# Performance work log

Measured on AMD Instinct MI355X. Metric: run time of the kernel, lower is better.

## Reference

```python
import jax, jax.numpy as jnp
import numpy as np

B, S, D, H = 1, 2048, 1024, 16
DEPTH = D // H          # 64
A_DFF = 1024
NRES = 2                # num_reslayerA
SLOPE = 0.2             # LeakyReLU slope in plga attention
POW_EPS = 1e-9


def _ln(x, g, b):
    m = jnp.mean(x, axis=-1, keepdims=True)
    v = jnp.var(x, axis=-1, keepdims=True)
    return (x - m) * jax.lax.rsqrt(v + 1e-6) * g + b


def setup_inputs() -> dict:
    key = jax.random.key(0)
    ks = jax.random.split(key, 12)
    s = 0.02
    W = lambda k, shp: jax.random.normal(k, shp, jnp.float32) * s
    return {
        'q': jax.random.normal(ks[0], (B, S, D), jnp.float32),
        'k': jax.random.normal(ks[1], (B, S, D), jnp.float32),
        'v': jax.random.normal(ks[2], (B, S, D), jnp.float32),
        'mask': jnp.zeros((B, 1, 1, S), jnp.float32),
        'wq_w': W(ks[3], (D, D)), 'wq_b': jnp.zeros((D,), jnp.float32),
        'wk_w': W(ks[4], (D, D)), 'wk_b': jnp.zeros((D,), jnp.float32),
        'wv_w': W(ks[5], (D, D)), 'wv_b': jnp.zeros((D,), jnp.float32),
        'wo_w': W(ks[6], (D, D)), 'wo_b': jnp.zeros((D,), jnp.float32),
        # stacked ResLayerA params: Dense(depth->A_dff, relu) -> Dense(A_dff->depth) -> LN
        'rl_w1': W(ks[7], (NRES, DEPTH, A_DFF)), 'rl_b1': jnp.zeros((NRES, A_DFF), jnp.float32),
        'rl_w2': W(ks[8], (NRES, A_DFF, DEPTH)), 'rl_b2': jnp.zeros((NRES, DEPTH), jnp.float32),
        'rl_g': jnp.ones((NRES, DEPTH), jnp.float32), 'rl_beta': jnp.zeros((NRES, DEPTH), jnp.float32),
        # plga layer params: power coefficients, attention vector, bias
        'pw': jnp.ones((DEPTH,), jnp.float32),
        'a_vec': W(ks[9], (DEPTH,)),
        'ba': jnp.zeros((), jnp.float32),
    }


def reference(q, k, v, mask, wq_w, wq_b, wk_w, wk_b, wv_w, wv_b, wo_w, wo_b,
              rl_w1, rl_b1, rl_w2, rl_b2, rl_g, rl_beta, pw, a_vec, ba):
    Bq = q.shape[0]
    split = lambda x: x.reshape(Bq, -1, H, DEPTH).transpose(0, 2, 1, 3)  # [b,h,s,d]
    qh = split(q @ wq_w + wq_b)
    kh = split(k @ wk_w + wk_b)
    vh = split(v @ wv_w + wv_b)

    # metric tensor A = q^T q  -> [b,h,depth,depth]
    A = jnp.einsum('bhsd,bhse->bhde', qh, qh)
    # ResLayerA residual dense+LN stack over last dim
    for i in range(NRES):
        Ain = A
        hdn = jax.nn.relu(A @ rl_w1[i] + rl_b1[i])
        A = _ln((hdn @ rl_w2[i] + rl_b2[i]) + Ain, rl_g[i], rl_beta[i])

    # power-law graph attention (plga_layer, att_head=1, activation=None)
    Ap = jnp.power(jnp.abs(A) + POW_EPS, pw)                  # element-wise learned power
    avAp = jnp.einsum('d,bhde->bhe', a_vec, Ap)               # [b,h,depth] per-dim scaling
    E = jnp.einsum('bhsd,bhd,bhtd->bhst', qh, avAp, kh)       # pairwise logits [b,h,s,s]
    Ep = jnp.where(E > 0, E, SLOPE * E) + ba                  # LeakyReLU + learned bias
    Ep = Ep + mask * (-1e9)
    attv = jax.nn.softmax(Ep, axis=-1)
    Hnext = jnp.einsum('bhst,bhtd->bhsd', attv, vh)

    Hnext = Hnext.transpose(0, 2, 1, 3).reshape(Bq, -1, D)
    out = Hnext @ wo_w + wo_b
    return (out, E, A, pw, attv, ba, avAp, Ep)
```

## Files before the change

### kernel.cpp

```cpp
#include <hip/hip_runtime.h>
#include <stdint.h>

#define S_ 2048
#define D_ 1024
#define H_ 16
#define DEP_ 64

typedef float f32x4 __attribute__((ext_vector_type(4)));
typedef __bf16 bf16x8 __attribute__((ext_vector_type(8)));

#define MFMA16(a,b,c) __builtin_amdgcn_mfma_f32_16x16x32_bf16((a),(b),(c),0,0,0)

static constexpr size_t OFF_E    = 2097152ull;
static constexpr size_t OFF_A    = 69206016ull;
static constexpr size_t OFF_PW   = 69271552ull;
static constexpr size_t OFF_ATT  = 69271616ull;
static constexpr size_t OFF_BA   = 136380480ull;
static constexpr size_t OFF_AVAP = 136380481ull;
static constexpr size_t OFF_EP   = 136381505ull;

__device__ __forceinline__ short f2b(float f) {
  union { float f; uint32_t u; } c; c.f = f;
  uint32_t u = c.u;
  uint32_t r = (u + 0x7fffu + ((u >> 16) & 1u)) >> 16;
  return (short)(r & 0xffffu);
}
__device__ __forceinline__ float b2f(short s) {
  union { uint32_t u; float f; } c; c.u = ((uint32_t)(uint16_t)s) << 16;
  return c.f;
}
__device__ __forceinline__ void st_nt(float* p, f32x4 v) {
  __builtin_nontemporal_store(v, (f32x4*)p);
}

__global__ void k_cvt_all(const float* __restrict__ q, const float* __restrict__ k,
                          const float* __restrict__ v, const float* __restrict__ wq,
                          const float* __restrict__ wk, const float* __restrict__ wv,
                          const float* __restrict__ wo, const float* __restrict__ w1,
                          const float* __restrict__ w2, short* __restrict__ xbf,
                          short* __restrict__ wT, short* __restrict__ w1T,
                          short* __restrict__ w2T) {
  __shared__ float tile[64][65];
  int bid = blockIdx.x, t = threadIdx.x;
  if (bid < 6144) {
    int z = bid >> 11, bx = bid & 2047;
    const float* src = (z == 0) ? q : (z == 1) ? k : v;
    short* d = xbf + (size_t)z * (S_*D_);
    int i = (bx*256 + t)*4;
    float4 f = *(const float4*)(src + i);
    short4 o;
    o.x = f2b(f.x); o.y = f2b(f.y); o.z = f2b(f.z); o.w = f2b(f.w);
    *(short4*)(d + i) = o;
  } else if (bid < 7168) {
    int u = bid - 6144, z = u >> 8, tl = u & 255;
    int k0 = (tl >> 4)*64, n0 = (tl & 15)*64;
    const float* W = (z == 0) ? wq : (z == 1) ? wk : (z == 2) ? wv : wo;
    short* d = wT + (size_t)z * (D_*D_);
    for (int i = 0; i < 16; ++i) {
      int e = i*256 + t, r = e >> 6, c = e & 63;
      tile[r][c] = W[(size_t)(k0+r)*D_ + n0 + c];
    }
    __syncthreads();
    for (int i = 0; i < 16; ++i) {
      int e = i*256 + t, r = e >> 6, c = e & 63;
      d[(size_t)(n0+r)*D_ + k0 + c] = f2b(tile[c][r]);
    }
  } else {
    int u = bid - 7168, z = u >> 4, bx = u & 15;
    int l = z >> 1, which = z & 1;
    if (which == 0) {
      const float* src = w1 + (size_t)l*65536;
      short* d = w1T + (size_t)l*65536;
      int n0 = bx*64;
      for (int i = 0; i < 16; ++i) {
        int e = i*256 + t, r = e >> 6, c = e & 63;
        tile[r][c] = src[(size_t)r*1024 + n0 + c];
      }
      __syncthreads();
      for (int i = 0; i < 16; ++i) {
        int e = i*256 + t, r = e >> 6, c = e & 63;
        d[(size_t)(n0+r)*64 + c] = f2b(tile[c][r]);
      }
    } else {
      const float* src = w2 + (size_t)l*65536;
      short* d = w2T + (size_t)l*65536;
      int k0 = bx*64;
      for (int i = 0; i < 16; ++i) {
        int e = i*256 + t, r = e >> 6, c = e & 63;
        tile[r][c] = src[(size_t)(k0+r)*64 + c];
      }
      __syncthreads();
      for (int i = 0; i < 16; ++i) {
        int e = i*256 + t, r = e >> 6, c = e & 63;
        d[(size_t)r*1024 + k0 + c] = f2b(tile[c][r]);
      }
    }
  }
}

__global__ __launch_bounds__(256) void k_gemm(
    const short* __restrict__ Xall, const short* __restrict__ X2,
    const short* __restrict__ WTall,
    const float* __restrict__ b0, const float* __restrict__ b1v,
    const float* __restrict__ b2v, short* __restrict__ dstall,
    float* __restrict__ outf, int mode) {
  __shared__ __align__(16) short SS[2*128*72];
  short* As = SS;
  short* Bs = SS + 128*72;
  int z = blockIdx.z;
  const short* X  = Xall + (size_t)z * (S_*D_);
  const short* WT = WTall + (size_t)z * (D_*D_);
  int m0 = blockIdx.x * 128, n0 = blockIdx.y * 128;
  int t = threadIdx.x, lane = t & 63;
  int wr = t >> 7, wc = (t >> 6) & 1;
  int rA = lane & 15, kg = lane >> 4;
  f32x4 acc[4][4] = {};
  for (int kt = 0; kt < 16; ++kt) {
#pragma unroll
    for (int i = 0; i < 4; ++i) {
      int cid = i*256 + t, row = cid >> 3, c = cid & 7;
      size_t xi = (size_t)(m0+row)*D_ + kt*64 + c*8;
      if (mode == 2) {
        union { int4 v; short s[8]; } a1, a2, o;
        a1.v = *(const int4*)&X[xi];
        a2.v = *(const int4*)&X2[xi];
#pragma unroll
        for (int j = 0; j < 8; ++j) o.s[j] = f2b(b2f(a1.s[j]) + b2f(a2.s[j]));
        *(int4*)&As[row*72 + c*8] = o.v;
      } else {
        *(int4*)&As[row*72 + c*8] = *(const int4*)&X[xi];
      }
      *(int4*)&Bs[row*72 + c*8] = *(const int4*)&WT[(size_t)(n0+row)*D_ + kt*64 + c*8];
    }
    __syncthreads();
#pragma unroll
    for (int kk = 0; kk < 2; ++kk) {
      bf16x8 a[4], b[4];
#pragma unroll
      for (int m = 0; m < 4; ++m)
        a[m] = *(const bf16x8*)&As[(wr*64 + m*16 + rA)*72 + kk*32 + kg*8];
#pragma unroll
      for (int n = 0; n < 4; ++n)
        b[n] = *(const bf16x8*)&Bs[(wc*64 + n*16 + rA)*72 + kk*32 + kg*8];
#pragma unroll
      for (int m = 0; m < 4; ++m)
#pragma unroll
        for (int n = 0; n < 4; ++n)
          acc[m][n] = MFMA16(a[m], b[n], acc[m][n]);
    }
    __syncthreads();
  }
  const float* bias = (mode != 0) ? b0 : (z == 0 ? b0 : (z == 1 ? b1v : b2v));
  if (mode == 0) {
    short* Ct = SS;
#pragma unroll
    for (int m = 0; m < 4; ++m)
#pragma unroll
      for (int n = 0; n < 4; ++n) {
        int col = wc*64 + n*16 + rA;
        float bb = bias[n0 + col];
#pragma unroll
        for (int rr = 0; rr < 4; ++rr) {
          int row = wr*64 + m*16 + kg*4 + rr;
          Ct[row*136 + col] = f2b(acc[m][n][rr] + bb);
        }
      }
    __syncthreads();
#pragma unroll
    for (int p = 0; p < 8; ++p) {
      int row = p*16 + (t >> 4), unit = t & 15;
      int4 vv = *(const int4*)&Ct[row*136 + unit*8];
      int gcol = n0 + unit*8;
      int head = gcol >> 6, dd = gcol & 63;
      *(int4*)&dstall[(size_t)z*(S_*D_) + ((size_t)head*S_ + m0 + row)*DEP_ + dd] = vv;
    }
  } else {
    float* Ct = (float*)SS;
#pragma unroll
    for (int half = 0; half < 2; ++half) {
      if (wr == half) {
#pragma unroll
        for (int m = 0; m < 4; ++m)
#pragma unroll
          for (int n = 0; n < 4; ++n) {
            int col = wc*64 + n*16 + rA;
            float bb = bias[n0 + col];
#pragma unroll
            for (int rr = 0; rr < 4; ++rr)
              Ct[(m*16 + kg*4 + rr)*132 + col] = acc[m][n][rr] + bb;
          }
      }
      __syncthreads();
#pragma unroll
      for (int p = 0; p < 8; ++p) {
        int row_l = p*8 + (t >> 5), unit = t & 31;
        f32x4 vv = *(const f32x4*)&Ct[row_l*132 + unit*4];
        st_nt(&outf[(size_t)(m0 + half*64 + row_l)*D_ + n0 + unit*4], vv);
      }
      __syncthreads();
    }
  }
}

__global__ void k_transpose(const short* __restrict__ qh, const short* __restrict__ vh,
                            short* __restrict__ qhT, short* __restrict__ vhT) {
  __shared__ short tile[64][68];
  const short* src = blockIdx.z ? vh : qh;
  short* dst = blockIdx.z ? vhT : qhT;
  int h = blockIdx.y, s0 = blockIdx.x * 64, t = threadIdx.x;
  for (int i = 0; i < 16; ++i) {
    int e = i*256 + t, r = e >> 6, c = e & 63;
    tile[r][c] = src[((size_t)h*S_ + s0 + r)*DEP_ + c];
  }
  __syncthreads();
  for (int i = 0; i < 16; ++i) {
    int e = i*256 + t, r = e >> 6, c = e & 63;
    dst[((size_t)h*DEP_ + r)*S_ + s0 + c] = tile[c][r];
  }
}

__global__ __launch_bounds__(256) void k_metric_p(const short* __restrict__ qhT,
                                                  float* __restrict__ Apart) {
  __shared__ short qt[64*72];
  int kc = blockIdx.x, h = blockIdx.y, t = threadIdx.x, lane = t & 63;
  int wr = t >> 7, wc = (t >> 6) & 1;
  int rA = lane & 15, kg = lane >> 4;
  f32x4 acc[2][2] = {};
  for (int kt = 0; kt < 4; ++kt) {
#pragma unroll
    for (int i = 0; i < 2; ++i) {
      int cid = i*256 + t, row = cid >> 3, c = cid & 7;
      *(int4*)&qt[row*72 + c*8] =
        *(const int4*)&qhT[((size_t)h*DEP_ + row)*S_ + kc*256 + kt*64 + c*8];
    }
    __syncthreads();
#pragma unroll
    for (int kk = 0; kk < 2; ++kk) {
      bf16x8 a[2], b[2];
#pragma unroll
      for (int m = 0; m < 2; ++m)
        a[m] = *(const bf16x8*)&qt[(wr*32 + m*16 + rA)*72 + kk*32 + kg*8];
#pragma unroll
      for (int n = 0; n < 2; ++n)
        b[n] = *(const bf16x8*)&qt[(wc*32 + n*16 + rA)*72 + kk*32 + kg*8];
#pragma unroll
      for (int m = 0; m < 2; ++m)
#pragma unroll
        for (int n = 0; n < 2; ++n)
          acc[m][n] = MFMA16(a[m], b[n], acc[m][n]);
    }
    __syncthreads();
  }
#pragma unroll
  for (int m = 0; m < 2; ++m)
#pragma unroll
    for (int n = 0; n < 2; ++n)
#pragma unroll
      for (int rr = 0; rr < 4; ++rr) {
        int row = wr*32 + m*16 + kg*4 + rr, col = wc*32 + n*16 + rA;
        Apart[((size_t)(kc*16 + h))*4096 + row*64 + col] = acc[m][n][rr];
      }
}

__global__ __launch_bounds__(512) void k_res(
    const float* __restrict__ Apart, const short* __restrict__ w1T,
    const float* __restrict__ b1, const short* __restrict__ w2T,
    const float* __restrict__ b2, const float* __restrict__ gl,
    const float* __restrict__ bel, const float* __restrict__ pwv,
    const float* __restrict__ av, const float* __restrict__ bav,
    float* __restrict__ avApW, float* __restrict__ outB) {
  __shared__ float Af[64][68];
  __shared__ short Afb[64][72];
  __shared__ short hdP[64*520];
  __shared__ float red[8][64];
  int h = blockIdx.x, t = threadIdx.x;
  int lane = t & 63, w = t >> 6;
  int rA = lane & 15, kg = lane >> 4;
#pragma unroll
  for (int i = 0; i < 2; ++i) {
    int idx = (i*512 + t)*4;
    f32x4 s = {};
#pragma unroll
    for (int kc = 0; kc < 8; ++kc)
      s += *(const f32x4*)&Apart[((size_t)(kc*16 + h))*4096 + idx];
    int r = idx >> 6, c = idx & 63;
    *(f32x4*)&Af[r][c] = s;
    union { int2 v; short sh[4]; } pk;
#pragma unroll
    for (int j = 0; j < 4; ++j) pk.sh[j] = f2b(s[j]);
    *(int2*)&Afb[r][c] = pk.v;
  }
  __syncthreads();
  for (int layer = 0; layer < 2; ++layer) {
    const short* w1l = w1T + layer*65536;
    const short* w2l = w2T + layer*65536;
    f32x4 acc2[4][4] = {};
    for (int kc = 0; kc < 2; ++kc) {
      int c0g = kc*512 + w*64;
      f32x4 acc1[4][4] = {};
#pragma unroll
      for (int kk = 0; kk < 2; ++kk) {
        bf16x8 aA[4], bW[4];
#pragma unroll
        for (int mf = 0; mf < 4; ++mf)
          aA[mf] = *(const bf16x8*)&Afb[mf*16 + rA][kk*32 + kg*8];
#pragma unroll
        for (int nf = 0; nf < 4; ++nf)
          bW[nf] = *(const bf16x8*)&w1l[(size_t)(c0g + nf*16 + rA)*64 + kk*32 + kg*8];
#pragma unroll
        for (int mf = 0; mf < 4; ++mf)
#pragma unroll
          for (int nf = 0; nf < 4; ++nf)
            acc1[mf][nf] = MFMA16(aA[mf], bW[nf], acc1[mf][nf]);
      }
      __syncthreads();
#pragma unroll
      for (int nf = 0; nf < 4; ++nf) {
        int col = w*64 + nf*16 + rA;
        float bb1 = b1[layer*1024 + kc*512 + col];
#pragma unroll
        for (int mf = 0; mf < 4; ++mf)
#pragma unroll
          for (int rr = 0; rr < 4; ++rr) {
            int r = mf*16 + kg*4 + rr;
            hdP[r*520 + col] = f2b(fmaxf(acc1[mf][nf][rr] + bb1, 0.f));
          }
      }
      __syncthreads();
#pragma unroll
      for (int kk = 0; kk < 2; ++kk) {
        bf16x8 a2[4], bw2[4];
#pragma unroll
        for (int mf = 0; mf < 4; ++mf)
          a2[mf] = *(const bf16x8*)&hdP[(mf*16 + rA)*520 + w*64 + kk*32 + kg*8];
#pragma unroll
        for (int nf = 0; nf < 4; ++nf)
          bw2[nf] = *(const bf16x8*)&w2l[(size_t)(nf*16 + rA)*1024 + kc*512 + w*64 + kk*32 + kg*8];
#pragma unroll
        for (int mf = 0; mf < 4; ++mf)
#pragma unroll
          for (int nf = 0; nf < 4; ++nf)
            acc2[mf][nf] = MFMA16(a2[mf], bw2[nf], acc2[mf][nf]);
      }
    }
    __syncthreads();
    float* P = (float*)hdP;
    if (w >= 4) {
      int slot = w - 4;
#pragma unroll
      for (int mf = 0; mf < 4; ++mf)
#pragma unroll
        for (int nf = 0; nf < 4; ++nf)
#pragma unroll
          for (int rr = 0; rr < 4; ++rr)
            P[slot*4160 + (mf*16 + kg*4 + rr)*65 + nf*16 + rA] = acc2[mf][nf][rr];
    }
    __syncthreads();
    if (w < 4) {
#pragma unroll
      for (int mf = 0; mf < 4; ++mf)
#pragma unroll
        for (int nf = 0; nf < 4; ++nf)
#pragma unroll
          for (int rr = 0; rr < 4; ++rr)
            P[w*4160 + (mf*16 + kg*4 + rr)*65 + nf*16 + rA] += acc2[mf][nf][rr];
    }
    __syncthreads();
    int r = t >> 3, j0 = (t & 7)*8;
    float x[8], s1 = 0.f, s2 = 0.f;
#pragma unroll
    for (int j = 0; j < 8; ++j) {
      int c = j0 + j;
      float xx = P[r*65 + c] + P[4160 + r*65 + c] + P[8320 + r*65 + c] + P[12480 + r*65 + c]
               + b2[layer*64 + c] + Af[r][c];
      x[j] = xx; s1 += xx; s2 += xx*xx;
    }
    s1 += __shfl_xor(s1, 1); s1 += __shfl_xor(s1, 2); s1 += __shfl_xor(s1, 4);
    s2 += __shfl_xor(s2, 1); s2 += __shfl_xor(s2, 2); s2 += __shfl_xor(s2, 4);
    float mean = s1 * (1.f/64.f);
    float var  = s2 * (1.f/64.f) - mean*mean;
    float rstd = rsqrtf(var + 1e-6f);
#pragma unroll
    for (int j = 0; j < 8; ++j) {
      int c = j0 + j;
      float nx = (x[j] - mean)*rstd*gl[layer*64 + c] + bel[layer*64 + c];
      Af[r][c] = nx;
      Afb[r][c] = f2b(nx);
      if (layer == 1) outB[OFF_A + (size_t)h*4096 + r*64 + c] = nx;
    }
    __syncthreads();
  }
  {
    int e = t & 63, dg = t >> 6;
    float pe = pwv[e], p = 0.f;
#pragma unroll
    for (int j = 0; j < 8; ++j) {
      int d = dg*8 + j;
      p += av[d] * powf(fabsf(Af[d][e]) + 1e-9f, pe);
    }
    red[dg][e] = p;
  }
  __syncthreads();
  if (t < 64) {
    float tot = 0.f;
#pragma unroll
    for (int g = 0; g < 8; ++g) tot += red[g][t];
    avApW[h*64 + t] = tot;
    outB[OFF_AVAP + h*64 + t] = tot;
  }
  if (h == 0) {
    if (t < 64) outB[OFF_PW + t] = pwv[t];
    if (t == 0) outB[OFF_BA] = bav[0];
  }
}

__global__ __launch_bounds__(256) void k_pass1(
    const short* __restrict__ qh, const short* __restrict__ kh,
    const float* __restrict__ avAp, const float* __restrict__ mask,
    const float* __restrict__ bap, float* __restrict__ outB,
    float2* __restrict__ part) {
  __shared__ float Et[64*128];
  __shared__ float avl[64];
  short* Qs = (short*)Et;
  short* Ks = ((short*)Et) + 8192;
  int tt = blockIdx.x, st = blockIdx.y, h = blockIdx.z;
  int s0 = st*128, t0 = tt*128;
  int t = threadIdx.x, lane = t & 63;
  int wr = t >> 7, wc = (t >> 6) & 1;
  int rA = lane & 15, kg = lane >> 4;
  if (t < 16) *(f32x4*)&avl[t*4] = *(const f32x4*)&avAp[h*64 + t*4];
  __syncthreads();
#pragma unroll
  for (int i = 0; i < 4; ++i) {
    int cid = i*256 + t, row = cid >> 3, c = cid & 7, cs = c ^ (row & 7);
    union { int4 v; short s[8]; } qa, qo;
    qa.v = *(const int4*)&qh[((size_t)h*S_ + s0 + row)*DEP_ + c*8];
#pragma unroll
    for (int j = 0; j < 8; ++j) qo.s[j] = f2b(b2f(qa.s[j]) * avl[c*8 + j]);
    *(int4*)&Qs[row*64 + cs*8] = qo.v;
    *(int4*)&Ks[row*64 + cs*8] = *(const int4*)&kh[((size_t)h*S_ + t0 + row)*DEP_ + c*8];
  }
  __syncthreads();
  f32x4 acc[4][4] = {};
#pragma unroll
  for (int kk = 0; kk < 2; ++kk) {
    bf16x8 a[4], b[4];
#pragma unroll
    for (int m = 0; m < 4; ++m) {
      int row = wr*64 + m*16 + rA, c = (kk*4 + kg) ^ (row & 7);
      a[m] = *(const bf16x8*)&Qs[row*64 + c*8];
    }
#pragma unroll
    for (int n = 0; n < 4; ++n) {
      int row = wc*64 + n*16 + rA, c = (kk*4 + kg) ^ (row & 7);
      b[n] = *(const bf16x8*)&Ks[row*64 + c*8];
    }
#pragma unroll
    for (int m = 0; m < 4; ++m)
#pragma unroll
      for (int n = 0; n < 4; ++n)
        acc[m][n] = MFMA16(b[n], a[m], acc[m][n]);
  }
  float bav = bap[0];
  f32x4 mkf[4];
#pragma unroll
  for (int n = 0; n < 4; ++n) {
    f32x4 mm = *(const f32x4*)&mask[t0 + wc*64 + n*16 + kg*4];
#pragma unroll
    for (int j = 0; j < 4; ++j) mkf[n][j] = mm[j] * (-1e9f);
  }
#pragma unroll
  for (int m = 0; m < 4; ++m) {
    int row = s0 + wr*64 + m*16 + rA;
    float mx = -3.4e38f;
    f32x4 ep4[4];
#pragma unroll
    for (int n = 0; n < 4; ++n) {
      f32x4 e = acc[m][n];
      f32x4 ep;
#pragma unroll
      for (int j = 0; j < 4; ++j) {
        float ee = e[j];
        ep[j] = (ee > 0.f ? ee : 0.2f*ee) + bav + mkf[n][j];
        mx = fmaxf(mx, ep[j]);
      }
      ep4[n] = ep;
    }
    mx = fmaxf(mx, __shfl_xor(mx, 16));
    mx = fmaxf(mx, __shfl_xor(mx, 32));
    float sm = 0.f;
#pragma unroll
    for (int n = 0; n < 4; ++n)
#pragma unroll
      for (int j = 0; j < 4; ++j) sm += expf(ep4[n][j] - mx);
    sm += __shfl_xor(sm, 16);
    sm += __shfl_xor(sm, 32);
    if (kg == 0)
      part[((size_t)(h*S_ + row)*16 + tt)*2 + wc] = make_float2(mx, sm);
  }
  float* Eo  = outB + OFF_E;
  float* Epo = outB + OFF_EP;
  int colu = t & 31, rbase = t >> 5;
  f32x4 mm4 = *(const f32x4*)&mask[t0 + colu*4];
  f32x4 mk4;
#pragma unroll
  for (int j = 0; j < 4; ++j) mk4[j] = mm4[j] * (-1e9f);
  __syncthreads();
#pragma unroll
  for (int half = 0; half < 2; ++half) {
    if (wr == half) {
#pragma unroll
      for (int m = 0; m < 4; ++m)
#pragma unroll
        for (int n = 0; n < 4; ++n) {
          int row_l = m*16 + rA;
          int unit = wc*16 + n*4 + kg;
          *(f32x4*)&Et[row_l*128 + ((unit ^ (row_l & 7)))*4] = acc[m][n];
        }
    }
    __syncthreads();
#pragma unroll
    for (int r = 0; r < 8; ++r) {
      int row_l = r*8 + rbase;
      f32x4 e = *(const f32x4*)&Et[row_l*128 + ((colu ^ (row_l & 7)))*4];
      size_t gb = ((size_t)h*S_ + s0 + half*64 + row_l)*S_ + t0 + colu*4;
      st_nt(&Eo[gb], e);
      f32x4 ep;
#pragma unroll
      for (int j = 0; j < 4; ++j)
        ep[j] = (e[j] > 0.f ? e[j] : 0.2f*e[j]) + bav + mk4[j];
      st_nt(&Epo[gb], ep);
    }
    __syncthreads();
  }
}

__global__ __launch_bounds__(256) void k_pass2(
    const short* __restrict__ qh, const short* __restrict__ kh,
    const short* __restrict__ vhT, const float* __restrict__ avAp,
    const float* __restrict__ mask, const float* __restrict__ bap,
    const float2* __restrict__ part, float* __restrict__ attv,
    short* __restrict__ Hnp0, short* __restrict__ Hnp1) {
  __shared__ short Qs[128*64];
  __shared__ __align__(16) short KP[128*128];
  __shared__ short Vs[64*128];
  __shared__ float avl[64];
  __shared__ float2 finS[128];
  int st = blockIdx.x, tc = blockIdx.y, h = blockIdx.z;
  int s0 = st * 128;
  int t = threadIdx.x, lane = t & 63;
  int wr = t >> 7, wc = (t >> 6) & 1;
  int rA = lane & 15, kg = lane >> 4;
  if (t < 16) *(f32x4*)&avl[t*4] = *(const f32x4*)&avAp[h*64 + t*4];
  if (t < 128) {
    const float2* pp = part + (size_t)(h*S_ + s0 + t) * 32;
    float M = -3.4e38f;
    for (int i = 0; i < 32; ++i) M = fmaxf(M, pp[i].x);
    float L = 0.f;
    for (int i = 0; i < 32; ++i) L += pp[i].y * expf(pp[i].x - M);
    finS[t] = make_float2(M, 1.f / L);
  }
  __syncthreads();
#pragma unroll
  for (int i = 0; i < 4; ++i) {
    int cid = i*256 + t, row = cid >> 3, c = cid & 7, cs = c ^ (row & 7);
    union { int4 v; short s[8]; } qa, qo;
    qa.v = *(const int4*)&qh[((size_t)h*S_ + s0 + row)*DEP_ + c*8];
#pragma unroll
    for (int j = 0; j < 8; ++j) qo.s[j] = f2b(b2f(qa.s[j]) * avl[c*8 + j]);
    *(int4*)&Qs[row*64 + cs*8] = qo.v;
  }
  float Ms[4], Li[4];
#pragma unroll
  for (int m = 0; m < 4; ++m) {
    float2 f = finS[wr*64 + m*16 + rA];
    Ms[m] = f.x; Li[m] = f.y;
  }
  float bav = bap[0];
  __syncthreads();
  bf16x8 aq[4][2];
#pragma unroll
  for (int m = 0; m < 4; ++m)
#pragma unroll
    for (int kk = 0; kk < 2; ++kk) {
      int row = wr*64 + m*16 + rA, c = (kk*4 + kg) ^ (row & 7);
      aq[m][kk] = *(const bf16x8*)&Qs[row*64 + c*8];
    }
  f32x4 acc2[4][2] = {};
  for (int tt = tc*8; tt < tc*8 + 8; ++tt) {
    int t0 = tt * 128;
    __syncthreads();
#pragma unroll
    for (int i = 0; i < 4; ++i) {
      int cid = i*256 + t, row = cid >> 3, c = cid & 7, cs = c ^ (row & 7);
      *(int4*)&KP[row*64 + cs*8] = *(const int4*)&kh[((size_t)h*S_ + t0 + row)*DEP_ + c*8];
    }
#pragma unroll
    for (int i = 0; i < 4; ++i) {
      int cid = i*256 + t, row = cid >> 4, c = cid & 15, cs = c ^ (row & 7);
      *(int4*)&Vs[row*128 + cs*8] = *(const int4*)&vhT[((size_t)h*DEP_ + row)*S_ + t0 + c*8];
    }
    __syncthreads();
    f32x4 accE[4][4] = {};
#pragma unroll
    for (int kk = 0; kk < 2; ++kk) {
      bf16x8 b[4];
#pragma unroll
      for (int n = 0; n < 4; ++n) {
        int row = wc*64 + n*16 + rA, c = (kk*4 + kg) ^ (row & 7);
        b[n] = *(const bf16x8*)&KP[row*64 + c*8];
      }
#pragma unroll
      for (int m = 0; m < 4; ++m)
#pragma unroll
        for (int n = 0; n < 4; ++n)
          accE[m][n] = MFMA16(b[n], aq[m][kk], accE[m][n]);
    }
    f32x4 mkf[4];
#pragma unroll
    for (int n = 0; n < 4; ++n) {
      f32x4 mm = *(const f32x4*)&mask[t0 + wc*64 + n*16 + kg*4];
#pragma unroll
      for (int j = 0; j < 4; ++j) mkf[n][j] = mm[j] * (-1e9f);
    }
#pragma unroll
    for (int m = 0; m < 4; ++m)
#pragma unroll
      for (int n = 0; n < 4; ++n) {
        f32x4 e = accE[m][n], p;
#pragma unroll
        for (int j = 0; j < 4; ++j) {
          float ep = (e[j] > 0.f ? e[j] : 0.2f*e[j]) + bav + mkf[n][j];
          p[j] = expf(ep - Ms[m]) * Li[m];
        }
        accE[m][n] = p;
      }
    __syncthreads();
#pragma unroll
    for (int m = 0; m < 4; ++m) {
      int srow = wr*64 + m*16 + rA;
#pragma unroll
      for (int n = 0; n < 4; ++n) {
        int tcol = wc*64 + n*16 + kg*4;
        union { int2 v; short s[4]; } pk;
#pragma unroll
        for (int j = 0; j < 4; ++j) pk.s[j] = f2b(accE[m][n][j]);
        *(int2*)((char*)KP + srow*256 + ((tcol*2) ^ ((srow & 7) << 4))) = pk.v;
      }
    }
    __syncthreads();
#pragma unroll
    for (int kkp = 0; kkp < 4; ++kkp) {
      bf16x8 ap[4], bv[2];
#pragma unroll
      for (int m = 0; m < 4; ++m) {
        int row = wr*64 + m*16 + rA;
        ap[m] = *(const bf16x8*)((const char*)KP + row*256 + ((kkp*64 + kg*16) ^ ((row & 7) << 4)));
      }
#pragma unroll
      for (int n = 0; n < 2; ++n) {
        int dd = wc*32 + n*16 + rA, c = (kkp*4 + kg) ^ (dd & 7);
        bv[n] = *(const bf16x8*)&Vs[dd*128 + c*8];
      }
#pragma unroll
      for (int m = 0; m < 4; ++m)
#pragma unroll
        for (int n = 0; n < 2; ++n)
          acc2[m][n] = MFMA16(ap[m], bv[n], acc2[m][n]);
    }
#pragma unroll
    for (int it = 0; it < 8; ++it) {
      int row = it*16 + (t >> 4);
      int unit = t & 15;
      union { int4 v; short s[8]; } pv;
      pv.v = *(const int4*)((const char*)KP + row*256 + ((unit*16) ^ ((row & 7) << 4)));
      f32x4 lo, hi;
#pragma unroll
      for (int j = 0; j < 4; ++j) { lo[j] = b2f(pv.s[j]); hi[j] = b2f(pv.s[4+j]); }
      size_t gb = ((size_t)h*S_ + s0 + row)*S_ + t0 + unit*8;
      st_nt(&attv[gb], lo);
      st_nt(&attv[gb + 4], hi);
    }
  }
  short* Hp = tc ? Hnp1 : Hnp0;
  short* Ht = KP;
  __syncthreads();
#pragma unroll
  for (int m = 0; m < 4; ++m)
#pragma unroll
    for (int n = 0; n < 2; ++n) {
      int col = wc*32 + n*16 + rA;
#pragma unroll
      for (int rr = 0; rr < 4; ++rr) {
        int row = wr*64 + m*16 + kg*4 + rr;
        Ht[row*72 + col] = f2b(acc2[m][n][rr]);
      }
    }
  __syncthreads();
#pragma unroll
  for (int p = 0; p < 4; ++p) {
    int row = p*32 + (t >> 3), unit = t & 7;
    int4 vv = *(const int4*)&Ht[row*72 + unit*8];
    *(int4*)&Hp[(size_t)(s0 + row)*D_ + h*DEP_ + unit*8] = vv;
  }
}

extern "C" void kernel_launch(void* const* d_in, const int* in_sizes, int n_in,
                              void* d_out, int out_size, void* d_ws, size_t ws_size,
                              hipStream_t stream) {
  (void)in_sizes; (void)n_in; (void)out_size; (void)ws_size;
  const float* q    = (const float*)d_in[0];
  const float* k    = (const float*)d_in[1];
  const float* v    = (const float*)d_in[2];
  const float* mask = (const float*)d_in[3];
  const float* wq_w = (const float*)d_in[4];
  const float* wq_b = (const float*)d_in[5];
  const float* wk_w = (const float*)d_in[6];
  const float* wk_b = (const float*)d_in[7];
  const float* wv_w = (const float*)d_in[8];
  const float* wv_b = (const float*)d_in[9];
  const float* wo_w = (const float*)d_in[10];
  const float* wo_b = (const float*)d_in[11];
  const float* rl_w1 = (const float*)d_in[12];
  const float* rl_b1 = (const float*)d_in[13];
  const float* rl_w2 = (const float*)d_in[14];
  const float* rl_b2 = (const float*)d_in[15];
  const float* rl_g  = (const float*)d_in[16];
  const float* rl_be = (const float*)d_in[17];
  const float* pw    = (const float*)d_in[18];
  const float* avec  = (const float*)d_in[19];
  const float* ba    = (const float*)d_in[20];
  float* outf = (float*)d_out;

  char* w = (char*)d_ws;
  short* xbf  = (short*)(w);
  short* wT   = (short*)(w + (12u << 20));
  short* qh   = (short*)(w + (20u << 20));
  short* kh   = (short*)(w + (24u << 20));
  short* vh   = (short*)(w + (28u << 20));
  short* qhT  = (short*)(w);
  short* vhT  = (short*)(w + (4u << 20));
  float* Apart = (float*)(w + (12u << 20));
  float2* part = (float2*)(w + (8u << 20));
  float* avApW = (float*)(w + (16u << 20) + (512u << 10));
  short* w1T  = (short*)(w + (32u << 20));
  short* w2T  = (short*)(w + (32u << 20) + (256u << 10));
  short* Hnp0 = (short*)(w);
  short* Hnp1 = (short*)(w + (28u << 20));

  k_cvt_all<<<dim3(7232), 256, 0, stream>>>(q, k, v, wq_w, wk_w, wv_w, wo_w,
                                            rl_w1, rl_w2, xbf, wT, w1T, w2T);
  k_gemm<<<dim3(16, 8, 3), 256, 0, stream>>>(xbf, nullptr, wT, wq_b, wk_b, wv_b,
                                             qh, nullptr, 0);
  k_transpose<<<dim3(32, 16, 2), 256, 0, stream>>>(qh, vh, qhT, vhT);
  k_metric_p<<<dim3(8, 16), 256, 0, stream>>>(qhT, Apart);
  k_res<<<dim3(16), 512, 0, stream>>>(Apart, w1T, rl_b1, w2T, rl_b2, rl_g, rl_be,
                                      pw, avec, ba, avApW, outf);
  k_pass1<<<dim3(16, 16, 16), 256, 0, stream>>>(qh, kh, avApW, mask, ba, outf, part);
  k_pass2<<<dim3(16, 2, 16), 256, 0, stream>>>(qh, kh, vhT, avApW, mask, ba, part,
                                               outf + OFF_ATT, Hnp0, Hnp1);
  k_gemm<<<dim3(16, 8, 1), 256, 0, stream>>>(Hnp0, Hnp1, wT + 3u*D_*D_,
                                             wo_b, wo_b, wo_b, nullptr, outf, 2);
}
```

Before: 475.0 us.

## Shrink pass1 tiles, split pass2 KV range four ways, add softmax stats reduce kernel

Pass1 now uses 64-row query tiles with four waves each covering 32 key columns. Per-row max and sum are combined in shared memory, so each block writes one partial per key tile instead of two. A new small kernel merges the 16 partials per row into final softmax statistics, so pass2 no longer redoes that reduction in every block. Pass2 splits the key range into four chunks instead of two, which doubles the block count, and writes four partial Hnext buffers that the output GEMM sums on load. The cost is an extra kernel launch, more workspace buffers, and more global reads in the final GEMM.

```diff
diff --git a/kernel.cpp b/kernel.cpp
--- a/kernel.cpp
+++ b/kernel.cpp
@@ -100,6 +100,7 @@
 
 __global__ __launch_bounds__(256) void k_gemm(
     const short* __restrict__ Xall, const short* __restrict__ X2,
+    const short* __restrict__ X3, const short* __restrict__ X4,
     const short* __restrict__ WTall,
     const float* __restrict__ b0, const float* __restrict__ b1v,
     const float* __restrict__ b2v, short* __restrict__ dstall,
@@ -121,11 +122,14 @@
       int cid = i*256 + t, row = cid >> 3, c = cid & 7;
       size_t xi = (size_t)(m0+row)*D_ + kt*64 + c*8;
       if (mode == 2) {
-        union { int4 v; short s[8]; } a1, a2, o;
+        union { int4 v; short s[8]; } a1, a2, a3, a4, o;
         a1.v = *(const int4*)&X[xi];
         a2.v = *(const int4*)&X2[xi];
-#pragma unroll
-        for (int j = 0; j < 8; ++j) o.s[j] = f2b(b2f(a1.s[j]) + b2f(a2.s[j]));
+        a3.v = *(const int4*)&X3[xi];
+        a4.v = *(const int4*)&X4[xi];
+#pragma unroll
+        for (int j = 0; j < 8; ++j)
+          o.s[j] = f2b(b2f(a1.s[j]) + b2f(a2.s[j]) + b2f(a3.s[j]) + b2f(a4.s[j]));
         *(int4*)&As[row*72 + c*8] = o.v;
       } else {
         *(int4*)&As[row*72 + c*8] = *(const int4*)&X[xi];
@@ -420,62 +424,65 @@
     const float* __restrict__ bap, float* __restrict__ outB,
     float2* __restrict__ part) {
   __shared__ float Et[64*128];
+  __shared__ float2 red[4][64];
   __shared__ float avl[64];
   short* Qs = (short*)Et;
-  short* Ks = ((short*)Et) + 8192;
-  int tt = blockIdx.x, st = blockIdx.y, h = blockIdx.z;
-  int s0 = st*128, t0 = tt*128;
-  int t = threadIdx.x, lane = t & 63;
-  int wr = t >> 7, wc = (t >> 6) & 1;
+  short* Ks = ((short*)Et) + 4096;
+  int tt = blockIdx.x, sb = blockIdx.y, h = blockIdx.z;
+  int s0 = sb*64, t0 = tt*128;
+  int t = threadIdx.x, lane = t & 63, w = t >> 6;
   int rA = lane & 15, kg = lane >> 4;
   if (t < 16) *(f32x4*)&avl[t*4] = *(const f32x4*)&avAp[h*64 + t*4];
   __syncthreads();
 #pragma unroll
-  for (int i = 0; i < 4; ++i) {
+  for (int i = 0; i < 6; ++i) {
     int cid = i*256 + t, row = cid >> 3, c = cid & 7, cs = c ^ (row & 7);
-    union { int4 v; short s[8]; } qa, qo;
-    qa.v = *(const int4*)&qh[((size_t)h*S_ + s0 + row)*DEP_ + c*8];
-#pragma unroll
-    for (int j = 0; j < 8; ++j) qo.s[j] = f2b(b2f(qa.s[j]) * avl[c*8 + j]);
-    *(int4*)&Qs[row*64 + cs*8] = qo.v;
-    *(int4*)&Ks[row*64 + cs*8] = *(const int4*)&kh[((size_t)h*S_ + t0 + row)*DEP_ + c*8];
-  }
-  __syncthreads();
-  f32x4 acc[4][4] = {};
+    if (row < 64) {
+      union { int4 v; short s[8]; } qa, qo;
+      qa.v = *(const int4*)&qh[((size_t)h*S_ + s0 + row)*DEP_ + c*8];
+#pragma unroll
+      for (int j = 0; j < 8; ++j) qo.s[j] = f2b(b2f(qa.s[j]) * avl[c*8 + j]);
+      *(int4*)&Qs[row*64 + cs*8] = qo.v;
+    } else {
+      int kr = row - 64, csk = c ^ (kr & 7);
+      *(int4*)&Ks[kr*64 + csk*8] = *(const int4*)&kh[((size_t)h*S_ + t0 + kr)*DEP_ + c*8];
+    }
+  }
+  __syncthreads();
+  f32x4 acc[4][2] = {};
 #pragma unroll
   for (int kk = 0; kk < 2; ++kk) {
-    bf16x8 a[4], b[4];
+    bf16x8 a[4], b[2];
 #pragma unroll
     for (int m = 0; m < 4; ++m) {
-      int row = wr*64 + m*16 + rA, c = (kk*4 + kg) ^ (row & 7);
+      int row = m*16 + rA, c = (kk*4 + kg) ^ (row & 7);
       a[m] = *(const bf16x8*)&Qs[row*64 + c*8];
     }
 #pragma unroll
-    for (int n = 0; n < 4; ++n) {
-      int row = wc*64 + n*16 + rA, c = (kk*4 + kg) ^ (row & 7);
-      b[n] = *(const bf16x8*)&Ks[row*64 + c*8];
+    for (int n = 0; n < 2; ++n) {
+      int kr = w*32 + n*16 + rA, c = (kk*4 + kg) ^ (kr & 7);
+      b[n] = *(const bf16x8*)&Ks[kr*64 + c*8];
     }
 #pragma unroll
     for (int m = 0; m < 4; ++m)
 #pragma unroll
-      for (int n = 0; n < 4; ++n)
+      for (int n = 0; n < 2; ++n)
         acc[m][n] = MFMA16(b[n], a[m], acc[m][n]);
   }
   float bav = bap[0];
-  f32x4 mkf[4];
-#pragma unroll
-  for (int n = 0; n < 4; ++n) {
-    f32x4 mm = *(const f32x4*)&mask[t0 + wc*64 + n*16 + kg*4];
+  f32x4 mkf[2];
+#pragma unroll
+  for (int n = 0; n < 2; ++n) {
+    f32x4 mm = *(const f32x4*)&mask[t0 + w*32 + n*16 + kg*4];
 #pragma unroll
     for (int j = 0; j < 4; ++j) mkf[n][j] = mm[j] * (-1e9f);
   }
 #pragma unroll
   for (int m = 0; m < 4; ++m) {
-    int row = s0 + wr*64 + m*16 + rA;
     float mx = -3.4e38f;
-    f32x4 ep4[4];
-#pragma unroll
-    for (int n = 0; n < 4; ++n) {
+    f32x4 ep4[2];
+#pragma unroll
+    for (int n = 0; n < 2; ++n) {
       f32x4 e = acc[m][n];
       f32x4 ep;
 #pragma unroll
@@ -490,14 +497,32 @@
     mx = fmaxf(mx, __shfl_xor(mx, 32));
     float sm = 0.f;
 #pragma unroll
-    for (int n = 0; n < 4; ++n)
+    for (int n = 0; n < 2; ++n)
 #pragma unroll
       for (int j = 0; j < 4; ++j) sm += expf(ep4[n][j] - mx);
     sm += __shfl_xor(sm, 16);
     sm += __shfl_xor(sm, 32);
-    if (kg == 0)
-      part[((size_t)(h*S_ + row)*16 + tt)*2 + wc] = make_float2(mx, sm);
-  }
+    if (kg == 0) red[w][m*16 + rA] = make_float2(mx, sm);
+  }
+  __syncthreads();
+  if (t < 64) {
+    float M = red[0][t].x;
+#pragma unroll
+    for (int g = 1; g < 4; ++g) M = fmaxf(M, red[g][t].x);
+    float L = 0.f;
+#pragma unroll
+    for (int g = 0; g < 4; ++g) L += red[g][t].y * expf(red[g][t].x - M);
+    part[((size_t)(h*S_ + s0 + t))*16 + tt] = make_float2(M, L);
+  }
+#pragma unroll
+  for (int m = 0; m < 4; ++m)
+#pragma unroll
+    for (int n = 0; n < 2; ++n) {
+      int row = m*16 + rA;
+      int unit = w*8 + n*4 + kg;
+      *(f32x4*)&Et[row*128 + ((unit ^ (row & 7)))*4] = acc[m][n];
+    }
+  __syncthreads();
   float* Eo  = outB + OFF_E;
   float* Epo = outB + OFF_EP;
   int colu = t & 31, rbase = t >> 5;
@@ -505,61 +530,50 @@
   f32x4 mk4;
 #pragma unroll
   for (int j = 0; j < 4; ++j) mk4[j] = mm4[j] * (-1e9f);
-  __syncthreads();
-#pragma unroll
-  for (int half = 0; half < 2; ++half) {
-    if (wr == half) {
-#pragma unroll
-      for (int m = 0; m < 4; ++m)
-#pragma unroll
-        for (int n = 0; n < 4; ++n) {
-          int row_l = m*16 + rA;
-          int unit = wc*16 + n*4 + kg;
-          *(f32x4*)&Et[row_l*128 + ((unit ^ (row_l & 7)))*4] = acc[m][n];
-        }
-    }
-    __syncthreads();
-#pragma unroll
-    for (int r = 0; r < 8; ++r) {
-      int row_l = r*8 + rbase;
-      f32x4 e = *(const f32x4*)&Et[row_l*128 + ((colu ^ (row_l & 7)))*4];
-      size_t gb = ((size_t)h*S_ + s0 + half*64 + row_l)*S_ + t0 + colu*4;
-      st_nt(&Eo[gb], e);
-      f32x4 ep;
-#pragma unroll
-      for (int j = 0; j < 4; ++j)
-        ep[j] = (e[j] > 0.f ? e[j] : 0.2f*e[j]) + bav + mk4[j];
-      st_nt(&Epo[gb], ep);
-    }
-    __syncthreads();
-  }
+#pragma unroll
+  for (int r = 0; r < 8; ++r) {
+    int row = r*8 + rbase;
+    f32x4 e = *(const f32x4*)&Et[row*128 + ((colu ^ (row & 7)))*4];
+    size_t gb = ((size_t)h*S_ + s0 + row)*S_ + t0 + colu*4;
+    st_nt(&Eo[gb], e);
+    f32x4 ep;
+#pragma unroll
+    for (int j = 0; j < 4; ++j)
+      ep[j] = (e[j] > 0.f ? e[j] : 0.2f*e[j]) + bav + mk4[j];
+    st_nt(&Epo[gb], ep);
+  }
+}
+
+__global__ void k_sreduce(const float2* __restrict__ part, float2* __restrict__ fin) {
+  int row = blockIdx.x * 256 + threadIdx.x;
+  const float2* pp = part + (size_t)row * 16;
+  float2 p[16];
+  float M = -3.4e38f;
+#pragma unroll
+  for (int i = 0; i < 16; ++i) { p[i] = pp[i]; M = fmaxf(M, p[i].x); }
+  float L = 0.f;
+#pragma unroll
+  for (int i = 0; i < 16; ++i) L += p[i].y * expf(p[i].x - M);
+  fin[row] = make_float2(M, L);
 }
 
 __global__ __launch_bounds__(256) void k_pass2(
     const short* __restrict__ qh, const short* __restrict__ kh,
     const short* __restrict__ vhT, const float* __restrict__ avAp,
     const float* __restrict__ mask, const float* __restrict__ bap,
-    const float2* __restrict__ part, float* __restrict__ attv,
-    short* __restrict__ Hnp0, short* __restrict__ Hnp1) {
+    const float2* __restrict__ fin, float* __restrict__ attv,
+    short* __restrict__ Hnp0, short* __restrict__ Hnp1,
+    short* __restrict__ Hnp2, short* __restrict__ Hnp3) {
   __shared__ short Qs[128*64];
   __shared__ __align__(16) short KP[128*128];
   __shared__ short Vs[64*128];
   __shared__ float avl[64];
-  __shared__ float2 finS[128];
   int st = blockIdx.x, tc = blockIdx.y, h = blockIdx.z;
   int s0 = st * 128;
   int t = threadIdx.x, lane = t & 63;
   int wr = t >> 7, wc = (t >> 6) & 1;
   int rA = lane & 15, kg = lane >> 4;
   if (t < 16) *(f32x4*)&avl[t*4] = *(const f32x4*)&avAp[h*64 + t*4];
-  if (t < 128) {
-    const float2* pp = part + (size_t)(h*S_ + s0 + t) * 32;
-    float M = -3.4e38f;
-    for (int i = 0; i < 32; ++i) M = fmaxf(M, pp[i].x);
-    float L = 0.f;
-    for (int i = 0; i < 32; ++i) L += pp[i].y * expf(pp[i].x - M);
-    finS[t] = make_float2(M, 1.f / L);
-  }
   __syncthreads();
 #pragma unroll
   for (int i = 0; i < 4; ++i) {
@@ -573,8 +587,8 @@
   float Ms[4], Li[4];
 #pragma unroll
   for (int m = 0; m < 4; ++m) {
-    float2 f = finS[wr*64 + m*16 + rA];
-    Ms[m] = f.x; Li[m] = f.y;
+    float2 f = fin[h*S_ + s0 + wr*64 + m*16 + rA];
+    Ms[m] = f.x; Li[m] = 1.f / f.y;
   }
   float bav = bap[0];
   __syncthreads();
@@ -587,7 +601,7 @@
       aq[m][kk] = *(const bf16x8*)&Qs[row*64 + c*8];
     }
   f32x4 acc2[4][2] = {};
-  for (int tt = tc*8; tt < tc*8 + 8; ++tt) {
+  for (int tt = tc*4; tt < tc*4 + 4; ++tt) {
     int t0 = tt * 128;
     __syncthreads();
 #pragma unroll
@@ -682,7 +696,7 @@
       st_nt(&attv[gb + 4], hi);
     }
   }
-  short* Hp = tc ? Hnp1 : Hnp0;
+  short* Hp = (tc == 0) ? Hnp0 : (tc == 1) ? Hnp1 : (tc == 2) ? Hnp2 : Hnp3;
   short* Ht = KP;
   __syncthreads();
 #pragma unroll
@@ -742,23 +756,27 @@
   short* vhT  = (short*)(w + (4u << 20));
   float* Apart = (float*)(w + (12u << 20));
   float2* part = (float2*)(w + (8u << 20));
+  float2* fin  = (float2*)(w + (16u << 20));
   float* avApW = (float*)(w + (16u << 20) + (512u << 10));
   short* w1T  = (short*)(w + (32u << 20));
   short* w2T  = (short*)(w + (32u << 20) + (256u << 10));
   short* Hnp0 = (short*)(w);
-  short* Hnp1 = (short*)(w + (28u << 20));
+  short* Hnp1 = (short*)(w + (12u << 20));
+  short* Hnp2 = (short*)(w + (28u << 20));
+  short* Hnp3 = (short*)(w + (8u << 20));
 
   k_cvt_all<<<dim3(7232), 256, 0, stream>>>(q, k, v, wq_w, wk_w, wv_w, wo_w,
                                             rl_w1, rl_w2, xbf, wT, w1T, w2T);
-  k_gemm<<<dim3(16, 8, 3), 256, 0, stream>>>(xbf, nullptr, wT, wq_b, wk_b, wv_b,
-                                             qh, nullptr, 0);
+  k_gemm<<<dim3(16, 8, 3), 256, 0, stream>>>(xbf, nullptr, nullptr, nullptr, wT,
+                                             wq_b, wk_b, wv_b, qh, nullptr, 0);
   k_transpose<<<dim3(32, 16, 2), 256, 0, stream>>>(qh, vh, qhT, vhT);
   k_metric_p<<<dim3(8, 16), 256, 0, stream>>>(qhT, Apart);
   k_res<<<dim3(16), 512, 0, stream>>>(Apart, w1T, rl_b1, w2T, rl_b2, rl_g, rl_be,
                                       pw, avec, ba, avApW, outf);
-  k_pass1<<<dim3(16, 16, 16), 256, 0, stream>>>(qh, kh, avApW, mask, ba, outf, part);
-  k_pass2<<<dim3(16, 2, 16), 256, 0, stream>>>(qh, kh, vhT, avApW, mask, ba, part,
-                                               outf + OFF_ATT, Hnp0, Hnp1);
-  k_gemm<<<dim3(16, 8, 1), 256, 0, stream>>>(Hnp0, Hnp1, wT + 3u*D_*D_,
+  k_pass1<<<dim3(16, 32, 16), 256, 0, stream>>>(qh, kh, avApW, mask, ba, outf, part);
+  k_sreduce<<<dim3(128), 256, 0, stream>>>(part, fin);
+  k_pass2<<<dim3(16, 4, 16), 256, 0, stream>>>(qh, kh, vhT, avApW, mask, ba, fin,
+                                               outf + OFF_ATT, Hnp0, Hnp1, Hnp2, Hnp3);
+  k_gemm<<<dim3(16, 8, 1), 256, 0, stream>>>(Hnp0, Hnp1, Hnp2, Hnp3, wT + 3u*D_*D_,
                                              wo_b, wo_b, wo_b, nullptr, outf, 2);
 }
```

After: 468.9 us. Within noise of the previous version (-1.3%).
